# Kernel tuning notes

Hardware: AMD Instinct MI355X
Metric: run time of the kernel (lower is better)

Reference implementation:

```python
import jax, jax.numpy as jnp
import numpy as np

S, B, N, K, D, H = 4, 8, 2048, 16, 32, 128


def setup_inputs() -> dict:
    key = jax.random.key(0)
    ks = jax.random.split(key, 7)
    x = jax.random.normal(ks[0], (S, B, N, D), dtype=jnp.float32)
    mu = jax.random.normal(ks[1], (S, B, K, D), dtype=jnp.float32)
    tau = jax.random.uniform(ks[2], (S, B, K, D), dtype=jnp.float32)  # precisions > 0
    # Linear(3D -> H); stored as (3D, H) i.e. transpose of torch's (H, 3D) weight
    W1 = jax.random.normal(ks[3], (3 * D, H), dtype=jnp.float32) * (1.0 / np.sqrt(3 * D))
    b1 = jax.random.normal(ks[4], (H,), dtype=jnp.float32) * 0.01
    W2 = jax.random.normal(ks[5], (H, 1), dtype=jnp.float32) * (1.0 / np.sqrt(H))
    b2 = jax.random.normal(ks[6], (1,), dtype=jnp.float32) * 0.01
    return {"x": x, "mu": mu, "tau": tau, "W1": W1, "b1": b1, "W2": W2, "b2": b2}


def reference(x, mu, tau, W1, b1, W2, b2):
    # Original torch code materializes var = cat([x_expand, mu_expand, tau_expand], -1)
    # of shape (S,B,N,K,3D) then applies Linear(3D,H). Mathematically identical:
    # split W1 rows into the x / mu / tau blocks and add the partial projections,
    # which avoids building the (S,B,N,K,3D) concat tensor.
    d = x.shape[-1]
    Wx, Wm, Wt = W1[:d], W1[d:2 * d], W1[2 * d:]
    hx = jnp.einsum('sbnd,dh->sbnh', x, Wx)                       # (S,B,N,H)
    hk = jnp.einsum('sbkd,dh->sbkh', mu, Wm) \
       + jnp.einsum('sbkd,dh->sbkh', tau, Wt)                     # (S,B,K,H)
    h = jnp.tanh(hx[:, :, :, None, :] + hk[:, :, None, :, :] + b1)  # (S,B,N,K,H)
    gamma = jnp.einsum('sbnkh,h->sbnk', h, W2[:, 0]) + b2[0]        # (S,B,N,K)
    q_probs = jax.nn.softmax(gamma, axis=-1)
    return q_probs
```

## Files before the change

### kernel.cpp

```cpp
#include <hip/hip_runtime.h>
#include <math.h>

typedef _Float16 half_t;
typedef __attribute__((ext_vector_type(8))) _Float16 half8;

#define EXP2F(x) __builtin_amdgcn_exp2f(x)
#define RCPF(x)  __builtin_amdgcn_rcpf(x)
#define C_SCALE 2.8853900817779268f

__global__ __launch_bounds__(512, 4) void fused_kernel(
    const float* __restrict__ x, const float* __restrict__ mu,
    const float* __restrict__ tau, const float* __restrict__ W1,
    const float* __restrict__ b1, const float* __restrict__ W2,
    float* __restrict__ out) {
  __shared__ __align__(16) float sX[128][36];
  __shared__ __align__(16) unsigned char sU[128 * 272];
  __shared__ __align__(16) float sEk[16][132];
  __shared__ __align__(16) float sW2[128];

  int t = threadIdx.x;
  int row0 = blockIdx.x * 128;
  int sb = row0 >> 11;

  const float4* x4 = (const float4*)(x + (size_t)row0 * 32);
#pragma unroll
  for (int i = 0; i < 2; ++i) {
    int j = i * 512 + t;
    int n = j >> 3, d4 = j & 7;
    float4 v = x4[j];
    v.x *= C_SCALE; v.y *= C_SCALE; v.z *= C_SCALE; v.w *= C_SCALE;
    *(float4*)&sX[n][d4 * 4] = v;
  }
#pragma unroll
  for (int i = 0; i < 2; ++i) {
    int j = i * 512 + t;
    int d = j >> 5, f = j & 31;
    *(float4*)(sU + d * 560 + f * 16 + (f >> 3) * 16) = ((const float4*)W1)[j];
  }
  if (t < 128) sW2[t] = -2.0f * W2[t];

  {
    int k = t >> 5, h0 = (t & 31) * 4;
    const float4* mu4  = (const float4*)(mu  + ((size_t)sb * 16 + k) * 32);
    const float4* tau4 = (const float4*)(tau + ((size_t)sb * 16 + k) * 32);
    float acc[4];
    {
      float4 ba = *(const float4*)(b1 + h0);
      acc[0] = ba.x; acc[1] = ba.y; acc[2] = ba.z; acc[3] = ba.w;
    }
    const float* Wm = W1 + 32 * 128 + h0;
    const float* Wt = W1 + 64 * 128 + h0;
#pragma unroll 2
    for (int d4 = 0; d4 < 8; ++d4) {
      float4 m4 = mu4[d4], t4 = tau4[d4];
      float mv4[4] = {m4.x, m4.y, m4.z, m4.w};
      float tv4[4] = {t4.x, t4.y, t4.z, t4.w};
#pragma unroll
      for (int dd = 0; dd < 4; ++dd) {
        int d = d4 * 4 + dd;
        float4 wm = *(const float4*)(Wm + d * 128);
        float4 wt = *(const float4*)(Wt + d * 128);
        float wmv[4] = {wm.x, wm.y, wm.z, wm.w};
        float wtv[4] = {wt.x, wt.y, wt.z, wt.w};
        float mv = mv4[dd], tv = tv4[dd];
#pragma unroll
        for (int l = 0; l < 4; ++l) {
          acc[l] = fmaf(mv, wmv[l], acc[l]);
          acc[l] = fmaf(tv, wtv[l], acc[l]);
        }
      }
    }
    float4 ev;
    ev.x = EXP2F(C_SCALE * acc[0]); ev.y = EXP2F(C_SCALE * acc[1]);
    ev.z = EXP2F(C_SCALE * acc[2]); ev.w = EXP2F(C_SCALE * acc[3]);
    *(float4*)&sEk[k][h0] = ev;
  }
  __syncthreads();

  int hg = t & 15, rg = t >> 4;
  int h0 = hg * 8, r0 = rg * 4;
  half8 hv[4];
  {
    const unsigned char* wbase = sU + hg * 32 + (hg >> 2) * 16;
    float acc[4][8];
#pragma unroll
    for (int j = 0; j < 4; ++j)
#pragma unroll
      for (int l = 0; l < 8; ++l) acc[j][l] = 0.f;
#pragma unroll 4
    for (int d = 0; d < 32; ++d) {
      float4 wa = *(const float4*)(wbase + d * 560);
      float4 wb = *(const float4*)(wbase + d * 560 + 16);
      float w[8] = {wa.x, wa.y, wa.z, wa.w, wb.x, wb.y, wb.z, wb.w};
#pragma unroll
      for (int j = 0; j < 4; ++j) {
        float xv = sX[r0 + j][d];
#pragma unroll
        for (int l = 0; l < 8; ++l) acc[j][l] = fmaf(xv, w[l], acc[j][l]);
      }
    }
#pragma unroll
    for (int j = 0; j < 4; ++j)
#pragma unroll
      for (int l = 0; l < 8; ++l) hv[j][l] = (half_t)EXP2F(acc[j][l]);
  }
  __syncthreads();

  half_t (*sEx)[136] = (half_t(*)[136])sU;
#pragma unroll
  for (int j = 0; j < 4; ++j) *(half8*)&sEx[r0 + j][h0] = hv[j];
  __syncthreads();

  int kg = t & 7, rg2 = t >> 3;
  int rp = rg2 * 2, k0 = kg * 2;
  const half_t* exr0 = &sEx[rp][0];
  const half_t* exr1 = &sEx[rp + 1][0];
  const float* ekr0 = &sEk[k0][0];
  const float* ekr1 = &sEk[k0 + 1][0];
  float a00 = 0.f, a01 = 0.f, a10 = 0.f, a11 = 0.f;
#pragma unroll
  for (int h8 = 0; h8 < 16; ++h8) {
    half8 ex0h = *(const half8*)(exr0 + h8 * 8);
    half8 ex1h = *(const half8*)(exr1 + h8 * 8);
    float4 f0a = *(const float4*)(ekr0 + h8 * 8);
    float4 f0b = *(const float4*)(ekr0 + h8 * 8 + 4);
    float4 f1a = *(const float4*)(ekr1 + h8 * 8);
    float4 f1b = *(const float4*)(ekr1 + h8 * 8 + 4);
    float4 wa  = *(const float4*)(&sW2[h8 * 8]);
    float4 wb  = *(const float4*)(&sW2[h8 * 8 + 4]);
    float e0[8], e1[8];
#pragma unroll
    for (int j = 0; j < 8; ++j) {
      e0[j] = (float)ex0h[j]; e1[j] = (float)ex1h[j];
    }
    float f0[8] = {f0a.x, f0a.y, f0a.z, f0a.w, f0b.x, f0b.y, f0b.z, f0b.w};
    float f1[8] = {f1a.x, f1a.y, f1a.z, f1a.w, f1b.x, f1b.y, f1b.z, f1b.w};
    float w[8]  = {wa.x, wa.y, wa.z, wa.w, wb.x, wb.y, wb.z, wb.w};
#pragma unroll
    for (int p = 0; p < 4; ++p) {
      int j0 = 2 * p, j1 = 2 * p + 1;
      {
        float A = fmaf(e0[j0], f0[j0], 1.f), B = fmaf(e0[j1], f0[j1], 1.f);
        a00 = fmaf(fmaf(w[j0], B, w[j1] * A), RCPF(A * B), a00);
      }
      {
        float A = fmaf(e0[j0], f1[j0], 1.f), B = fmaf(e0[j1], f1[j1], 1.f);
        a01 = fmaf(fmaf(w[j0], B, w[j1] * A), RCPF(A * B), a01);
      }
      {
        float A = fmaf(e1[j0], f0[j0], 1.f), B = fmaf(e1[j1], f0[j1], 1.f);
        a10 = fmaf(fmaf(w[j0], B, w[j1] * A), RCPF(A * B), a10);
      }
      {
        float A = fmaf(e1[j0], f1[j0], 1.f), B = fmaf(e1[j1], f1[j1], 1.f);
        a11 = fmaf(fmaf(w[j0], B, w[j1] * A), RCPF(A * B), a11);
      }
    }
  }

  const float l2e = 1.4426950408889634f;
  {
    float m = fmaxf(a00, a01);
#pragma unroll
    for (int s = 1; s < 8; s <<= 1) m = fmaxf(m, __shfl_xor(m, s, 8));
    float p0 = EXP2F((a00 - m) * l2e), p1 = EXP2F((a01 - m) * l2e);
    float sum = p0 + p1;
#pragma unroll
    for (int s = 1; s < 8; s <<= 1) sum += __shfl_xor(sum, s, 8);
    float inv = RCPF(sum);
    float2 o = make_float2(p0 * inv, p1 * inv);
    *(float2*)&out[(size_t)(row0 + rp) * 16 + k0] = o;
  }
  {
    float m = fmaxf(a10, a11);
#pragma unroll
    for (int s = 1; s < 8; s <<= 1) m = fmaxf(m, __shfl_xor(m, s, 8));
    float p0 = EXP2F((a10 - m) * l2e), p1 = EXP2F((a11 - m) * l2e);
    float sum = p0 + p1;
#pragma unroll
    for (int s = 1; s < 8; s <<= 1) sum += __shfl_xor(sum, s, 8);
    float inv = RCPF(sum);
    float2 o = make_float2(p0 * inv, p1 * inv);
    *(float2*)&out[(size_t)(row0 + rp + 1) * 16 + k0] = o;
  }
}

extern "C" void kernel_launch(void* const* d_in, const int* in_sizes, int n_in,
                              void* d_out, int out_size, void* d_ws, size_t ws_size,
                              hipStream_t stream) {
  const float* x   = (const float*)d_in[0];
  const float* mu  = (const float*)d_in[1];
  const float* tau = (const float*)d_in[2];
  const float* W1  = (const float*)d_in[3];
  const float* b1  = (const float*)d_in[4];
  const float* W2  = (const float*)d_in[5];
  float* out = (float*)d_out;
  (void)in_sizes; (void)n_in; (void)out_size; (void)d_ws; (void)ws_size;

  fused_kernel<<<512, 512, 0, stream>>>(x, mu, tau, W1, b1, W2, out);
}
```

Measured before the change: 98.25 us.

## Split per-(s,b) mu/tau projection into a prep kernel; vectorize x loads

Moves the mu/tau projection and its exp2 into a separate prep kernel that writes a half-precision table to workspace. The main kernel then loads that table instead of recomputing it, since before each of the 16 blocks sharing an (s,b) pair redid the same work. The x-projection loop now reads x from shared memory as float4 vectors per four d values. The cost is an extra kernel launch, a dependency through global memory, and fp16 rounding of the k-side exp values.

Measured after the change: 93.14 us. -5.2%, faster.

```diff
diff --git a/kernel.cpp b/kernel.cpp
--- a/kernel.cpp
+++ b/kernel.cpp
@@ -3,15 +3,32 @@
 
 typedef _Float16 half_t;
 typedef __attribute__((ext_vector_type(8))) _Float16 half8;
+typedef __attribute__((ext_vector_type(4))) _Float16 half4;
 
 #define EXP2F(x) __builtin_amdgcn_exp2f(x)
 #define RCPF(x)  __builtin_amdgcn_rcpf(x)
 #define C_SCALE 2.8853900817779268f
 
-__global__ __launch_bounds__(512, 4) void fused_kernel(
-    const float* __restrict__ x, const float* __restrict__ mu,
-    const float* __restrict__ tau, const float* __restrict__ W1,
-    const float* __restrict__ b1, const float* __restrict__ W2,
+__global__ __launch_bounds__(256) void prep_kernel(
+    const float* __restrict__ mu, const float* __restrict__ tau,
+    const float* __restrict__ W1, const float* __restrict__ b1,
+    half_t* __restrict__ ek) {
+  int g = blockIdx.x * 256 + threadIdx.x;
+  int h = g & 127, row = g >> 7;
+  const float* mur  = mu  + row * 32;
+  const float* taur = tau + row * 32;
+  float acc = b1[h];
+#pragma unroll
+  for (int d = 0; d < 32; ++d) {
+    acc = fmaf(mur[d],  W1[(32 + d) * 128 + h], acc);
+    acc = fmaf(taur[d], W1[(64 + d) * 128 + h], acc);
+  }
+  ek[g] = (half_t)EXP2F(C_SCALE * acc);
+}
+
+__global__ __launch_bounds__(512, 4) void main_kernel(
+    const float* __restrict__ x, const float* __restrict__ W1,
+    const float* __restrict__ W2, const half_t* __restrict__ ek,
     float* __restrict__ out) {
   __shared__ __align__(16) float sX[128][36];
   __shared__ __align__(16) unsigned char sU[128 * 272];
@@ -21,6 +38,16 @@
   int t = threadIdx.x;
   int row0 = blockIdx.x * 128;
   int sb = row0 >> 11;
+
+  {
+    int k = t >> 5, h0 = (t & 31) * 4;
+    half4 ev = *(const half4*)(ek + (size_t)sb * 2048 + k * 128 + h0);
+    float4 f;
+    f.x = (float)ev[0]; f.y = (float)ev[1];
+    f.z = (float)ev[2]; f.w = (float)ev[3];
+    *(float4*)&sEk[k][h0] = f;
+  }
+  if (t < 128) sW2[t] = -2.0f * W2[t];
 
   const float4* x4 = (const float4*)(x + (size_t)row0 * 32);
 #pragma unroll
@@ -37,44 +64,6 @@
     int d = j >> 5, f = j & 31;
     *(float4*)(sU + d * 560 + f * 16 + (f >> 3) * 16) = ((const float4*)W1)[j];
   }
-  if (t < 128) sW2[t] = -2.0f * W2[t];
-
-  {
-    int k = t >> 5, h0 = (t & 31) * 4;
-    const float4* mu4  = (const float4*)(mu  + ((size_t)sb * 16 + k) * 32);
-    const float4* tau4 = (const float4*)(tau + ((size_t)sb * 16 + k) * 32);
-    float acc[4];
-    {
-      float4 ba = *(const float4*)(b1 + h0);
-      acc[0] = ba.x; acc[1] = ba.y; acc[2] = ba.z; acc[3] = ba.w;
-    }
-    const float* Wm = W1 + 32 * 128 + h0;
-    const float* Wt = W1 + 64 * 128 + h0;
-#pragma unroll 2
-    for (int d4 = 0; d4 < 8; ++d4) {
-      float4 m4 = mu4[d4], t4 = tau4[d4];
-      float mv4[4] = {m4.x, m4.y, m4.z, m4.w};
-      float tv4[4] = {t4.x, t4.y, t4.z, t4.w};
-#pragma unroll
-      for (int dd = 0; dd < 4; ++dd) {
-        int d = d4 * 4 + dd;
-        float4 wm = *(const float4*)(Wm + d * 128);
-        float4 wt = *(const float4*)(Wt + d * 128);
-        float wmv[4] = {wm.x, wm.y, wm.z, wm.w};
-        float wtv[4] = {wt.x, wt.y, wt.z, wt.w};
-        float mv = mv4[dd], tv = tv4[dd];
-#pragma unroll
-        for (int l = 0; l < 4; ++l) {
-          acc[l] = fmaf(mv, wmv[l], acc[l]);
-          acc[l] = fmaf(tv, wtv[l], acc[l]);
-        }
-      }
-    }
-    float4 ev;
-    ev.x = EXP2F(C_SCALE * acc[0]); ev.y = EXP2F(C_SCALE * acc[1]);
-    ev.z = EXP2F(C_SCALE * acc[2]); ev.w = EXP2F(C_SCALE * acc[3]);
-    *(float4*)&sEk[k][h0] = ev;
-  }
   __syncthreads();
 
   int hg = t & 15, rg = t >> 4;
@@ -87,16 +76,26 @@
     for (int j = 0; j < 4; ++j)
 #pragma unroll
       for (int l = 0; l < 8; ++l) acc[j][l] = 0.f;
-#pragma unroll 4
-    for (int d = 0; d < 32; ++d) {
-      float4 wa = *(const float4*)(wbase + d * 560);
-      float4 wb = *(const float4*)(wbase + d * 560 + 16);
-      float w[8] = {wa.x, wa.y, wa.z, wa.w, wb.x, wb.y, wb.z, wb.w};
+#pragma unroll
+    for (int d4 = 0; d4 < 8; ++d4) {
+      float xc[4][4];
 #pragma unroll
       for (int j = 0; j < 4; ++j) {
-        float xv = sX[r0 + j][d];
-#pragma unroll
-        for (int l = 0; l < 8; ++l) acc[j][l] = fmaf(xv, w[l], acc[j][l]);
+        float4 xv = *(const float4*)&sX[r0 + j][d4 * 4];
+        xc[j][0] = xv.x; xc[j][1] = xv.y; xc[j][2] = xv.z; xc[j][3] = xv.w;
+      }
+#pragma unroll
+      for (int dd = 0; dd < 4; ++dd) {
+        int d = d4 * 4 + dd;
+        float4 wa = *(const float4*)(wbase + d * 560);
+        float4 wb = *(const float4*)(wbase + d * 560 + 16);
+        float w[8] = {wa.x, wa.y, wa.z, wa.w, wb.x, wb.y, wb.z, wb.w};
+#pragma unroll
+        for (int j = 0; j < 4; ++j) {
+          float xv = xc[j][dd];
+#pragma unroll
+          for (int l = 0; l < 8; ++l) acc[j][l] = fmaf(xv, w[l], acc[j][l]);
+        }
       }
     }
 #pragma unroll
@@ -195,7 +194,10 @@
   const float* b1  = (const float*)d_in[4];
   const float* W2  = (const float*)d_in[5];
   float* out = (float*)d_out;
-  (void)in_sizes; (void)n_in; (void)out_size; (void)d_ws; (void)ws_size;
-
-  fused_kernel<<<512, 512, 0, stream>>>(x, mu, tau, W1, b1, W2, out);
+
+  half_t* ek = (half_t*)d_ws;
+  (void)in_sizes; (void)n_in; (void)out_size; (void)ws_size;
+
+  prep_kernel<<<256, 256, 0, stream>>>(mu, tau, W1, b1, ek);
+  main_kernel<<<512, 512, 0, stream>>>(x, W1, W2, ek, out);
 }
```

## Stage Wm/Wt in shared memory, store Ek and W2 as fp16, vectorize x reads

Applied to the files above, without the earlier changes.

The Wm/Wt weight blocks are copied into shared memory once and the per-cluster projection is computed by 256 threads, each handling two clusters, instead of every thread reading W1 from global memory. The exp(hk) table and the scaled W2 are stored as fp16, which halves their LDS footprint and the number of read instructions in the inner pairwise loop. The x-projection loop now loads sX as float4 and reuses it across four d steps. In exchange, a larger 69KB shared buffer may lower occupancy, and fp16 storage of Ek and W2 adds rounding error.

Result: faster. 91.42 us (-7.0%).

```diff
diff --git a/kernel.cpp b/kernel.cpp
--- a/kernel.cpp
+++ b/kernel.cpp
@@ -3,6 +3,7 @@
 
 typedef _Float16 half_t;
 typedef __attribute__((ext_vector_type(8))) _Float16 half8;
+typedef __attribute__((ext_vector_type(4))) _Float16 half4;
 
 #define EXP2F(x) __builtin_amdgcn_exp2f(x)
 #define RCPF(x)  __builtin_amdgcn_rcpf(x)
@@ -13,10 +14,13 @@
     const float* __restrict__ tau, const float* __restrict__ W1,
     const float* __restrict__ b1, const float* __restrict__ W2,
     float* __restrict__ out) {
-  __shared__ __align__(16) float sX[128][36];
-  __shared__ __align__(16) unsigned char sU[128 * 272];
-  __shared__ __align__(16) float sEk[16][132];
-  __shared__ __align__(16) float sW2[128];
+  __shared__ __align__(16) unsigned char sA[69120];
+  __shared__ __align__(16) half_t sEk[16][136];
+  __shared__ __align__(16) half_t sW2[128];
+
+  float (*sX)[36] = (float(*)[36])sA;
+  unsigned char* sW = sA + 18432;
+  float* sWmt = (float*)(sA + 36352);
 
   int t = threadIdx.x;
   int row0 = blockIdx.x * 128;
@@ -35,26 +39,48 @@
   for (int i = 0; i < 2; ++i) {
     int j = i * 512 + t;
     int d = j >> 5, f = j & 31;
-    *(float4*)(sU + d * 560 + f * 16 + (f >> 3) * 16) = ((const float4*)W1)[j];
-  }
-  if (t < 128) sW2[t] = -2.0f * W2[t];
-
-  {
-    int k = t >> 5, h0 = (t & 31) * 4;
-    const float4* mu4  = (const float4*)(mu  + ((size_t)sb * 16 + k) * 32);
-    const float4* tau4 = (const float4*)(tau + ((size_t)sb * 16 + k) * 32);
-    float acc[4];
+    *(float4*)(sW + d * 560 + f * 16 + (f >> 3) * 16) = ((const float4*)W1)[j];
+  }
+  {
+    const float4* wmt4 = (const float4*)(W1 + 32 * 128);
+    float4* dst = (float4*)sWmt;
+#pragma unroll
+    for (int i = 0; i < 4; ++i) dst[i * 512 + t] = wmt4[i * 512 + t];
+  }
+  if (t < 16) {
+    float4 a = ((const float4*)W2)[2 * t];
+    float4 b = ((const float4*)W2)[2 * t + 1];
+    half8 hv;
+    hv[0] = (half_t)(-2.f * a.x); hv[1] = (half_t)(-2.f * a.y);
+    hv[2] = (half_t)(-2.f * a.z); hv[3] = (half_t)(-2.f * a.w);
+    hv[4] = (half_t)(-2.f * b.x); hv[5] = (half_t)(-2.f * b.y);
+    hv[6] = (half_t)(-2.f * b.z); hv[7] = (half_t)(-2.f * b.w);
+    *(half8*)&sW2[t * 8] = hv;
+  }
+  __syncthreads();
+
+  if (t < 256) {
+    int k0 = (t >> 5) * 2, h0 = (t & 31) * 4;
+    const float4* mu4a  = (const float4*)(mu  + ((size_t)sb * 16 + k0) * 32);
+    const float4* tau4a = (const float4*)(tau + ((size_t)sb * 16 + k0) * 32);
+    const float4* mu4b  = mu4a + 8;
+    const float4* tau4b = tau4a + 8;
+    float acc0[4], acc1[4];
     {
       float4 ba = *(const float4*)(b1 + h0);
-      acc[0] = ba.x; acc[1] = ba.y; acc[2] = ba.z; acc[3] = ba.w;
-    }
-    const float* Wm = W1 + 32 * 128 + h0;
-    const float* Wt = W1 + 64 * 128 + h0;
+      acc0[0] = ba.x; acc0[1] = ba.y; acc0[2] = ba.z; acc0[3] = ba.w;
+      acc1[0] = ba.x; acc1[1] = ba.y; acc1[2] = ba.z; acc1[3] = ba.w;
+    }
+    const float* Wm = sWmt + h0;
+    const float* Wt = sWmt + 32 * 128 + h0;
 #pragma unroll 2
     for (int d4 = 0; d4 < 8; ++d4) {
-      float4 m4 = mu4[d4], t4 = tau4[d4];
-      float mv4[4] = {m4.x, m4.y, m4.z, m4.w};
-      float tv4[4] = {t4.x, t4.y, t4.z, t4.w};
+      float4 ma = mu4a[d4], ta = tau4a[d4];
+      float4 mb = mu4b[d4], tb = tau4b[d4];
+      float mva[4] = {ma.x, ma.y, ma.z, ma.w};
+      float tva[4] = {ta.x, ta.y, ta.z, ta.w};
+      float mvb[4] = {mb.x, mb.y, mb.z, mb.w};
+      float tvb[4] = {tb.x, tb.y, tb.z, tb.w};
 #pragma unroll
       for (int dd = 0; dd < 4; ++dd) {
         int d = d4 * 4 + dd;
@@ -62,41 +88,55 @@
         float4 wt = *(const float4*)(Wt + d * 128);
         float wmv[4] = {wm.x, wm.y, wm.z, wm.w};
         float wtv[4] = {wt.x, wt.y, wt.z, wt.w};
-        float mv = mv4[dd], tv = tv4[dd];
 #pragma unroll
         for (int l = 0; l < 4; ++l) {
-          acc[l] = fmaf(mv, wmv[l], acc[l]);
-          acc[l] = fmaf(tv, wtv[l], acc[l]);
+          acc0[l] = fmaf(mva[dd], wmv[l], acc0[l]);
+          acc0[l] = fmaf(tva[dd], wtv[l], acc0[l]);
+          acc1[l] = fmaf(mvb[dd], wmv[l], acc1[l]);
+          acc1[l] = fmaf(tvb[dd], wtv[l], acc1[l]);
         }
       }
     }
-    float4 ev;
-    ev.x = EXP2F(C_SCALE * acc[0]); ev.y = EXP2F(C_SCALE * acc[1]);
-    ev.z = EXP2F(C_SCALE * acc[2]); ev.w = EXP2F(C_SCALE * acc[3]);
-    *(float4*)&sEk[k][h0] = ev;
-  }
-  __syncthreads();
+    half4 h0v, h1v;
+#pragma unroll
+    for (int l = 0; l < 4; ++l) {
+      h0v[l] = (half_t)EXP2F(C_SCALE * acc0[l]);
+      h1v[l] = (half_t)EXP2F(C_SCALE * acc1[l]);
+    }
+    *(half4*)&sEk[k0][h0] = h0v;
+    *(half4*)&sEk[k0 + 1][h0] = h1v;
+  }
 
   int hg = t & 15, rg = t >> 4;
   int h0 = hg * 8, r0 = rg * 4;
   half8 hv[4];
   {
-    const unsigned char* wbase = sU + hg * 32 + (hg >> 2) * 16;
+    const unsigned char* wbase = sW + hg * 32 + (hg >> 2) * 16;
     float acc[4][8];
 #pragma unroll
     for (int j = 0; j < 4; ++j)
 #pragma unroll
       for (int l = 0; l < 8; ++l) acc[j][l] = 0.f;
-#pragma unroll 4
-    for (int d = 0; d < 32; ++d) {
-      float4 wa = *(const float4*)(wbase + d * 560);
-      float4 wb = *(const float4*)(wbase + d * 560 + 16);
-      float w[8] = {wa.x, wa.y, wa.z, wa.w, wb.x, wb.y, wb.z, wb.w};
+#pragma unroll
+    for (int d4 = 0; d4 < 8; ++d4) {
+      float xc[4][4];
 #pragma unroll
       for (int j = 0; j < 4; ++j) {
-        float xv = sX[r0 + j][d];
-#pragma unroll
-        for (int l = 0; l < 8; ++l) acc[j][l] = fmaf(xv, w[l], acc[j][l]);
+        float4 xv = *(const float4*)&sX[r0 + j][d4 * 4];
+        xc[j][0] = xv.x; xc[j][1] = xv.y; xc[j][2] = xv.z; xc[j][3] = xv.w;
+      }
+#pragma unroll
+      for (int dd = 0; dd < 4; ++dd) {
+        int d = d4 * 4 + dd;
+        float4 wa = *(const float4*)(wbase + d * 560);
+        float4 wb = *(const float4*)(wbase + d * 560 + 16);
+        float w[8] = {wa.x, wa.y, wa.z, wa.w, wb.x, wb.y, wb.z, wb.w};
+#pragma unroll
+        for (int j = 0; j < 4; ++j) {
+          float xv = xc[j][dd];
+#pragma unroll
+          for (int l = 0; l < 8; ++l) acc[j][l] = fmaf(xv, w[l], acc[j][l]);
+        }
       }
     }
 #pragma unroll
@@ -106,7 +146,7 @@
   }
   __syncthreads();
 
-  half_t (*sEx)[136] = (half_t(*)[136])sU;
+  half_t (*sEx)[136] = (half_t(*)[136])sA;
 #pragma unroll
   for (int j = 0; j < 4; ++j) *(half8*)&sEx[r0 + j][h0] = hv[j];
   __syncthreads();
@@ -115,27 +155,23 @@
   int rp = rg2 * 2, k0 = kg * 2;
   const half_t* exr0 = &sEx[rp][0];
   const half_t* exr1 = &sEx[rp + 1][0];
-  const float* ekr0 = &sEk[k0][0];
-  const float* ekr1 = &sEk[k0 + 1][0];
+  const half_t* ekr0 = &sEk[k0][0];
+  const half_t* ekr1 = &sEk[k0 + 1][0];
   float a00 = 0.f, a01 = 0.f, a10 = 0.f, a11 = 0.f;
 #pragma unroll
   for (int h8 = 0; h8 < 16; ++h8) {
     half8 ex0h = *(const half8*)(exr0 + h8 * 8);
     half8 ex1h = *(const half8*)(exr1 + h8 * 8);
-    float4 f0a = *(const float4*)(ekr0 + h8 * 8);
-    float4 f0b = *(const float4*)(ekr0 + h8 * 8 + 4);
-    float4 f1a = *(const float4*)(ekr1 + h8 * 8);
-    float4 f1b = *(const float4*)(ekr1 + h8 * 8 + 4);
-    float4 wa  = *(const float4*)(&sW2[h8 * 8]);
-    float4 wb  = *(const float4*)(&sW2[h8 * 8 + 4]);
-    float e0[8], e1[8];
+    half8 ek0h = *(const half8*)(ekr0 + h8 * 8);
+    half8 ek1h = *(const half8*)(ekr1 + h8 * 8);
+    half8 wvh  = *(const half8*)(&sW2[h8 * 8]);
+    float e0[8], e1[8], f0[8], f1[8], w[8];
 #pragma unroll
     for (int j = 0; j < 8; ++j) {
       e0[j] = (float)ex0h[j]; e1[j] = (float)ex1h[j];
-    }
-    float f0[8] = {f0a.x, f0a.y, f0a.z, f0a.w, f0b.x, f0b.y, f0b.z, f0b.w};
-    float f1[8] = {f1a.x, f1a.y, f1a.z, f1a.w, f1b.x, f1b.y, f1b.z, f1b.w};
-    float w[8]  = {wa.x, wa.y, wa.z, wa.w, wb.x, wb.y, wb.z, wb.w};
+      f0[j] = (float)ek0h[j]; f1[j] = (float)ek1h[j];
+      w[j]  = (float)wvh[j];
+    }
 #pragma unroll
     for (int p = 0; p < 4; ++p) {
       int j0 = 2 * p, j1 = 2 * p + 1;
```
